# Optimization experiments

Hardware: AMD Instinct MI355X
Metric: run time of the kernel (lower is better)

Reference implementation:

```python
import jax, jax.numpy as jnp
import numpy as np

B, A = 4096, 8          # episodes, agents per episode
N = B * A               # total nodes
E = B * A * (A - 1)     # fully-connected directed edges within each group
F_IN, D, H, M, NA = 64, 64, 4, 64, 10  # in_feat, gnn_dim, heads, mem_dim, n_actions
NEG_SLOPE = 0.2
LN_EPS = 1e-5


def _build_edge_index():
    base = np.arange(A)
    s = np.repeat(base, A)
    d = np.tile(base, A)
    keep = s != d
    s, d = s[keep], d[keep]                       # [A*(A-1)]
    offs = (np.arange(B) * A)[:, None]
    src = (offs + s[None, :]).reshape(-1)
    dst = (offs + d[None, :]).reshape(-1)
    return jnp.asarray(np.stack([src, dst]), dtype=jnp.int32)  # [2, E]


def setup_inputs() -> dict:
    key = jax.random.key(0)
    ks = jax.random.split(key, 16)
    sc = 0.05
    return {
        "x": jax.random.normal(ks[0], (N, F_IN), jnp.float32),
        "edge_attr": jax.random.normal(ks[1], (E, 3), jnp.float32),
        "hidden": jax.random.normal(ks[2], (N, M), jnp.float32) * sc,
        "edge_index": _build_edge_index(),
        # GATv2 params
        "Wl": jax.random.normal(ks[3], (H * D, F_IN), jnp.float32) * sc,
        "bl": jnp.zeros((H * D,), jnp.float32),
        "Wr": jax.random.normal(ks[4], (H * D, F_IN), jnp.float32) * sc,
        "br": jnp.zeros((H * D,), jnp.float32),
        "We": jax.random.normal(ks[5], (H * D, 3), jnp.float32) * sc,
        "be": jnp.zeros((H * D,), jnp.float32),
        "att": jax.random.normal(ks[6], (H, D), jnp.float32) * sc,
        "bias_g": jnp.zeros((D,), jnp.float32),
        # GRUCell params (gate order r,z,n as in torch)
        "W_ih": jax.random.normal(ks[7], (3 * M, D), jnp.float32) * sc,
        "W_hh": jax.random.normal(ks[8], (3 * M, M), jnp.float32) * sc,
        "b_ih": jnp.zeros((3 * M,), jnp.float32),
        "b_hh": jnp.zeros((3 * M,), jnp.float32),
        # LayerNorm + output Linear
        "ln_g": jnp.ones((M,), jnp.float32),
        "ln_b": jnp.zeros((M,), jnp.float32),
        "Wq": jax.random.normal(ks[9], (NA, M), jnp.float32) * sc,
        "bq": jnp.zeros((NA,), jnp.float32),
    }


def reference(x, edge_attr, hidden, edge_index, Wl, bl, Wr, br, We, be, att,
              bias_g, W_ih, W_hh, b_ih, b_hh, ln_g, ln_b, Wq, bq):
    src, dst = edge_index[0], edge_index[1]
    # GATv2Conv (concat=False -> mean over heads), share_weights=False
    xl = (x @ Wl.T + bl).reshape(N, H, D)          # source projection
    xr = (x @ Wr.T + br).reshape(N, H, D)          # target projection
    ee = (edge_attr @ We.T + be).reshape(E, H, D)  # edge embedding
    m = jax.nn.leaky_relu(xl[src] + xr[dst] + ee, NEG_SLOPE)  # [E,H,D]
    logits = jnp.einsum('ehd,hd->eh', m, att)                  # [E,H]
    lmax = jax.ops.segment_max(logits, dst, num_segments=N)    # [N,H]
    ex = jnp.exp(logits - lmax[dst])
    denom = jax.ops.segment_sum(ex, dst, num_segments=N)       # [N,H]
    alpha = ex / denom[dst]                                    # softmax per target
    agg = jax.ops.segment_sum(alpha[:, :, None] * xl[src], dst, num_segments=N)  # [N,H,D]
    h_gnn = jax.nn.relu(agg.mean(axis=1) + bias_g)             # [N,D]
    # GRUCell
    gi = h_gnn @ W_ih.T + b_ih
    gh = hidden @ W_hh.T + b_hh
    ir, iz, inn = jnp.split(gi, 3, axis=-1)
    hr, hz, hn = jnp.split(gh, 3, axis=-1)
    r = jax.nn.sigmoid(ir + hr)
    z = jax.nn.sigmoid(iz + hz)
    n = jnp.tanh(inn + r * hn)
    h = (1.0 - z) * n + z * hidden                              # [N,M]
    # LayerNorm + Linear head
    mu = h.mean(axis=-1, keepdims=True)
    var = ((h - mu) ** 2).mean(axis=-1, keepdims=True)
    hln = (h - mu) / jnp.sqrt(var + LN_EPS) * ln_g + ln_b
    q = hln @ Wq.T + bq                                         # [N,NA]
    return q, h
```

## Files before the change

kernel.cpp:

```cpp
#include <hip/hip_runtime.h>

typedef unsigned short u16;
typedef unsigned int u32;
typedef __attribute__((ext_vector_type(8))) short bf16x8;
typedef __attribute__((ext_vector_type(4))) float f32x4;
typedef _Float16 f16;
typedef __attribute__((ext_vector_type(2))) f16 h2;
typedef __attribute__((ext_vector_type(8))) f16 h8;

#define NAG 8
#define NAGB 16
#define FIN 64
#define MDIM 64
#define NACT 10
#define EPG 56
#define NTOT 32768
#define ABP 72
#define XLS 272
#define XHS 64

#define U_XR  4352
#define U_RZ  0
#define U_HNH 4224
#define U_INB 5312
#define U_HG  6400
#define U_LN  3200

__device__ __forceinline__ float b2f(u16 u) {
  return __uint_as_float(((unsigned int)u) << 16);
}
__device__ __forceinline__ u16 f2b(float f) {
  unsigned int x = __float_as_uint(f);
  unsigned int r = x + 0x7fffu + ((x >> 16) & 1u);
  return (u16)(r >> 16);
}
__device__ __forceinline__ u16 f2h(float f) {
  f16 h = (f16)f; u16 u; __builtin_memcpy(&u, &h, 2); return u;
}
__device__ __forceinline__ float h2f(u16 u) {
  f16 h; __builtin_memcpy(&h, &u, 2); return (float)h;
}
__device__ __forceinline__ u32 pkh2(float a, float b) {
#if __has_builtin(__builtin_amdgcn_cvt_pkrtz)
  auto r = __builtin_amdgcn_cvt_pkrtz(a, b);
  u32 u; __builtin_memcpy(&u, &r, 4); return u;
#else
  return (u32)f2h(a) | ((u32)f2h(b) << 16);
#endif
}

union H8u { h8 v; h2 p[4]; };

__device__ __forceinline__ h8 lrelu8(h8 m) {
  h8 s = m * (f16)0.2f;
#if __has_builtin(__builtin_elementwise_max)
  return __builtin_elementwise_max(m, s);
#else
  h8 r;
#pragma unroll
  for (int i = 0; i < 8; i++) r[i] = (m[i] > s[i]) ? m[i] : s[i];
  return r;
#endif
}

#if __has_builtin(__builtin_amdgcn_fdot2)
__device__ __forceinline__ float dotacc(h2 a, h2 b, float c) {
  return __builtin_amdgcn_fdot2(a, b, c, false);
}
#else
__device__ __forceinline__ float dotacc(h2 a, h2 b, float c) {
  c += (float)a[0] * (float)b[0];
  c += (float)a[1] * (float)b[1];
  return c;
}
#endif

__global__ __launch_bounds__(256) void prep_weights(
    const float* __restrict__ Wl, const float* __restrict__ Wr,
    const float* __restrict__ Wih, const float* __restrict__ Whh,
    u16* __restrict__ wsB)
{
  const int idx = blockIdx.x * 256 + threadIdx.x;
  if (idx >= 56 * 2 * 64) return;
  const int L  = idx & 63;
  const int ks = (idx >> 6) & 1;
  const int T  = idx >> 7;
  const float* W; int row0;
  if      (T < 16) { W = Wl;  row0 = T * 16; }
  else if (T < 32) { W = Wr;  row0 = (T - 16) * 16; }
  else if (T < 44) { W = Wih; row0 = (T - 32) * 16; }
  else             { W = Whh; row0 = (T - 44) * 16; }
  const int row = row0 + (L & 15);
  const int k0  = ks * 32 + (L >> 4) * 8;
  u16 v[8];
#pragma unroll
  for (int j = 0; j < 8; j++) v[j] = f2b(W[row * 64 + k0 + j]);
  *(bf16x8*)(wsB + (size_t)idx * 8) = *(bf16x8*)v;
}

__global__ __launch_bounds__(256, 7) void gnn_rnn_kernel(
    const float* __restrict__ x, const float* __restrict__ edge_attr,
    const float* __restrict__ hidden,
    const float* __restrict__ bl, const float* __restrict__ br,
    const float* __restrict__ We, const float* __restrict__ be,
    const float* __restrict__ att, const float* __restrict__ bias_g,
    const float* __restrict__ b_ih, const float* __restrict__ b_hh,
    const float* __restrict__ ln_g, const float* __restrict__ ln_b,
    const float* __restrict__ Wq, const float* __restrict__ bq,
    const u16* __restrict__ wsB,
    float* __restrict__ d_out)
{
  __shared__ __align__(16) char uraw[17408];
  __shared__ __align__(16) u16 s_al[NAGB * 4 * 8];
  __shared__ __align__(16) u16 s_hidb[NAGB * ABP];
  __shared__ __align__(16) u16 s_w0h[256], s_w1h[256], s_w2h[256], s_atth[256];

  u16*   uXL  = (u16*)uraw;
  u16*   uXR  = (u16*)uraw + U_XR;
  u16*   uHn  = (u16*)uraw + U_HNH;
  u16*   uInn = (u16*)uraw + U_INB;
  u16*   s_hgb = (u16*)uraw + U_HG;
  float* uF   = (float*)uraw;
  u16*   s_xb = (u16*)uraw;

  const int t = threadIdx.x;
  const int b = blockIdx.x;
  const int L = t & 63;
  const int w = t >> 6;
  const int q = L >> 4;

  {
    const float* xb = x + b * (NAGB * FIN);
    const float* hb = hidden + b * (NAGB * MDIM);
#pragma unroll
    for (int i = t; i < NAGB * FIN; i += 256) {
      const int a = i >> 6, m = i & 63;
      s_xb[a * ABP + m] = f2b(xb[i]);
      s_hidb[a * ABP + m] = f2b(hb[i]);
    }
    s_w0h[t]  = f2h(We[t * 3]);
    s_w1h[t]  = f2h(We[t * 3 + 1]);
    s_w2h[t]  = f2h(We[t * 3 + 2]);
    s_atth[t] = f2h(att[t]);
  }
  float ea00 = 0.f, ea01 = 0.f, ea02 = 0.f, ea10 = 0.f, ea11 = 0.f, ea12 = 0.f;
  if (L < EPG) {
    const float* eb = edge_attr + b * (2 * EPG * 3) + L * 3;
    ea00 = eb[0]; ea01 = eb[1]; ea02 = eb[2];
    ea10 = eb[EPG * 3]; ea11 = eb[EPG * 3 + 1]; ea12 = eb[EPG * 3 + 2];
  }
  __syncthreads();

  {
    const int arow = L & 15;
    bf16x8 af0 = *(const bf16x8*)&s_xb[arow * ABP + q * 8];
    bf16x8 af1 = *(const bf16x8*)&s_xb[arow * ABP + 32 + q * 8];
    __syncthreads();
    const bf16x8* wsBv = (const bf16x8*)wsB;
#pragma unroll 4
    for (int i = 0; i < 8; i++) {
      const int T = w * 8 + i;
      f32x4 acc = {0.f, 0.f, 0.f, 0.f};
      acc = __builtin_amdgcn_mfma_f32_16x16x32_bf16(wsBv[(T * 2 + 0) * 64 + L], af0, acc, 0, 0, 0);
      acc = __builtin_amdgcn_mfma_f32_16x16x32_bf16(wsBv[(T * 2 + 1) * 64 + L], af1, acc, 0, 0, 0);
      const int agent = L & 15;
      const int Tm = T & 15;
      const int h = Tm >> 2;
      const int gcb = Tm * 16 + q * 4;
      const int d0 = (Tm & 3) * 16 + q * 4;
      f32x4 bias4;
      if (T < 16) bias4 = *(const f32x4*)(bl + gcb);
      else        bias4 = *(const f32x4*)(br + gcb) + *(const f32x4*)(be + gcb);
      f32x4 v = acc + bias4;
      u32 pk2[2] = { pkh2(v[0], v[1]), pkh2(v[2], v[3]) };
      u16* dst = (T < 16 ? uXL : uXR) + agent * XLS + h * XHS + d0;
      *(uint2*)dst = *(uint2*)pk2;
    }
  }
  __syncthreads();

  {
    const int h = w;
    if (L < EPG) {
      const int e = L;
      const int s = e / 7, k = e % 7;
      const int j = k + (k >= s ? 1 : 0);
      const f16 a00 = (f16)ea00, a01 = (f16)ea01, a02 = (f16)ea02;
      const f16 a10 = (f16)ea10, a11 = (f16)ea11, a12 = (f16)ea12;
      const u16* xlp0 = uXL + s * XLS + h * XHS;
      const u16* xrp0 = uXR + j * XLS + h * XHS;
      const u16* xlp1 = uXL + (8 + s) * XLS + h * XHS;
      const u16* xrp1 = uXR + (8 + j) * XLS + h * XHS;
      const u16* w0p = s_w0h + h * 64;
      const u16* w1p = s_w1h + h * 64;
      const u16* w2p = s_w2h + h * 64;
      const u16* atp = s_atth + h * 64;
      float lgA0 = 0.f, lgB0 = 0.f, lgA1 = 0.f, lgB1 = 0.f;
#pragma unroll 2
      for (int kq = 0; kq < 8; kq++) {
        H8u w0, w1, w2, at, x0, r0, x1, r1, m0, m1;
        w0.v = *(const h8*)(w0p + kq * 8);
        w1.v = *(const h8*)(w1p + kq * 8);
        w2.v = *(const h8*)(w2p + kq * 8);
        at.v = *(const h8*)(atp + kq * 8);
        x0.v = *(const h8*)(xlp0 + kq * 8);
        r0.v = *(const h8*)(xrp0 + kq * 8);
        x1.v = *(const h8*)(xlp1 + kq * 8);
        r1.v = *(const h8*)(xrp1 + kq * 8);
        m0.v = x0.v + r0.v + w0.v * a00 + w1.v * a01 + w2.v * a02;
        m0.v = lrelu8(m0.v);
        m1.v = x1.v + r1.v + w0.v * a10 + w1.v * a11 + w2.v * a12;
        m1.v = lrelu8(m1.v);
        lgA0 = dotacc(m0.p[0], at.p[0], lgA0);
        lgB0 = dotacc(m0.p[1], at.p[1], lgB0);
        lgA0 = dotacc(m0.p[2], at.p[2], lgA0);
        lgB0 = dotacc(m0.p[3], at.p[3], lgB0);
        lgA1 = dotacc(m1.p[0], at.p[0], lgA1);
        lgB1 = dotacc(m1.p[1], at.p[1], lgB1);
        lgA1 = dotacc(m1.p[2], at.p[2], lgA1);
        lgB1 = dotacc(m1.p[3], at.p[3], lgB1);
      }
      s_al[((    j) * 4 + h) * 8 + s] = f2h(__expf(lgA0 + lgB0));
      s_al[((8 + j) * 4 + h) * 8 + s] = f2h(__expf(lgA1 + lgB1));
    } else {
      const int j2 = L - EPG;
      s_al[((    j2) * 4 + w) * 8 + j2] = 0;
      s_al[((8 + j2) * 4 + w) * 8 + j2] = 0;
    }
  }
  __syncthreads();

  {
    const int ep = t >> 7, jj = (t >> 4) & 7, dq = t & 15;
    const int a16 = ep * 8 + jj;
    float acc[4] = {0.f, 0.f, 0.f, 0.f};
#pragma unroll
    for (int h = 0; h < 4; h++) {
      H8u av;
      av.v = *(const h8*)&s_al[(a16 * 4 + h) * 8];
      float den = 0.f;
      float ah[4] = {0.f, 0.f, 0.f, 0.f};
#pragma unroll
      for (int s = 0; s < 8; s++) {
        float al = (float)av.v[s];
        den += al;
        const u16* xp = uXL + (ep * 8 + s) * XLS + h * XHS + dq * 4;
        ushort4 xv = *(const ushort4*)xp;
        ah[0] += al * h2f(xv.x);
        ah[1] += al * h2f(xv.y);
        ah[2] += al * h2f(xv.z);
        ah[3] += al * h2f(xv.w);
      }
      const float inv = 1.f / den;
#pragma unroll
      for (int c = 0; c < 4; c++) acc[c] += ah[c] * inv;
    }
    const f32x4 bg = *(const f32x4*)(bias_g + dq * 4);
    u16 pk[4];
#pragma unroll
    for (int c = 0; c < 4; c++) {
      float v = acc[c] * 0.25f + bg[c];
      pk[c] = f2b(v > 0.f ? v : 0.f);
    }
    *(uint2*)&s_hgb[a16 * ABP + dq * 4] = *(uint2*)pk;
  }
  __syncthreads();

  {
    const int arow = L & 15;
    bf16x8 ag0 = *(const bf16x8*)&s_hgb[arow * ABP + q * 8];
    bf16x8 ag1 = *(const bf16x8*)&s_hgb[arow * ABP + 32 + q * 8];
    bf16x8 ah0 = *(const bf16x8*)&s_hidb[arow * ABP + q * 8];
    bf16x8 ah1 = *(const bf16x8*)&s_hidb[arow * ABP + 32 + q * 8];
    const bf16x8* wsBv = (const bf16x8*)wsB;
#pragma unroll
    for (int i = 0; i < 3; i++) {
      const int T6 = w * 3 + i;
      const int Tg = 32 + T6, Th = 44 + T6;
      f32x4 acci = {0.f, 0.f, 0.f, 0.f};
      acci = __builtin_amdgcn_mfma_f32_16x16x32_bf16(wsBv[(Tg * 2 + 0) * 64 + L], ag0, acci, 0, 0, 0);
      acci = __builtin_amdgcn_mfma_f32_16x16x32_bf16(wsBv[(Tg * 2 + 1) * 64 + L], ag1, acci, 0, 0, 0);
      f32x4 acch = {0.f, 0.f, 0.f, 0.f};
      acch = __builtin_amdgcn_mfma_f32_16x16x32_bf16(wsBv[(Th * 2 + 0) * 64 + L], ah0, acch, 0, 0, 0);
      acch = __builtin_amdgcn_mfma_f32_16x16x32_bf16(wsBv[(Th * 2 + 1) * 64 + L], ah1, acch, 0, 0, 0);
      const int agent = L & 15;
      const int gcb = T6 * 16 + q * 4;
      if (T6 < 8) {
        f32x4 bsum = *(const f32x4*)(b_ih + gcb) + *(const f32x4*)(b_hh + gcb);
        f32x4 v = acci + acch + bsum;
        *(f32x4*)&uF[U_RZ + agent * 132 + gcb] = v;
      } else {
        f32x4 vi = acci + *(const f32x4*)(b_ih + gcb);
        f32x4 vh = acch + *(const f32x4*)(b_hh + gcb);
        const int off = agent * 68 + (gcb - 128);
        u32 pi[2] = { pkh2(vi[0], vi[1]), pkh2(vi[2], vi[3]) };
        u32 ph[2] = { pkh2(vh[0], vh[1]), pkh2(vh[2], vh[3]) };
        *(uint2*)&uInn[off] = *(uint2*)pi;
        *(uint2*)&uHn[off]  = *(uint2*)ph;
      }
    }
  }
  __syncthreads();

  {
    const float lng = ln_g[L];
    const float lnb = ln_b[L];
#pragma unroll
    for (int rr = 0; rr < 4; rr++) {
      const int a = w + rr * 4, m = L;
      float rz_r = uF[U_RZ + a * 132 + m];
      float rz_z = uF[U_RZ + a * 132 + 64 + m];
      float inn  = h2f(uInn[a * 68 + m]);
      float hn   = h2f(uHn[a * 68 + m]);
      float hid  = b2f(s_hidb[a * ABP + m]);
      float r = 1.f / (1.f + __expf(-rz_r));
      float z = 1.f / (1.f + __expf(-rz_z));
      float xg = inn + r * hn;
      xg = fminf(fmaxf(xg, -20.f), 20.f);
      float e2 = __expf(2.f * xg);
      float n = (e2 - 1.f) / (e2 + 1.f);
      float hv = (1.f - z) * n + z * hid;
      d_out[NTOT * NACT + (b * NAGB + a) * MDIM + m] = hv;
      float sum = hv, sq = hv * hv;
#pragma unroll
      for (int off = 1; off < 64; off <<= 1) {
        sum += __shfl_xor(sum, off, 64);
        sq  += __shfl_xor(sq,  off, 64);
      }
      float mu  = sum * (1.f / 64.f);
      float var = sq * (1.f / 64.f) - mu * mu;
      var = var > 0.f ? var : 0.f;
      uF[U_LN + a * 68 + m] = (hv - mu) * rsqrtf(var + 1e-5f) * lng + lnb;
    }
  }
  __syncthreads();

  if (t < NAGB * NACT) {
    const int a = t / NACT, o = t % NACT;
    float acc = bq[o];
    const float4* lv = (const float4*)(uF + U_LN + a * 68);
    const float4* wv = (const float4*)(Wq + o * 64);
#pragma unroll 4
    for (int kq = 0; kq < 16; kq++) {
      float4 l4 = lv[kq], w4 = wv[kq];
      acc += l4.x * w4.x + l4.y * w4.y + l4.z * w4.z + l4.w * w4.w;
    }
    d_out[(b * NAGB + a) * NACT + o] = acc;
  }
}

extern "C" void kernel_launch(void* const* d_in, const int* in_sizes, int n_in,
                              void* d_out, int out_size, void* d_ws, size_t ws_size,
                              hipStream_t stream) {
  const int N  = in_sizes[0] / FIN;
  const int Bn = N / NAGB;
  u16* wsB = (u16*)d_ws;

  prep_weights<<<28, 256, 0, stream>>>(
      (const float*)d_in[4],
      (const float*)d_in[6],
      (const float*)d_in[12],
      (const float*)d_in[13],
      wsB);

  gnn_rnn_kernel<<<Bn, 256, 0, stream>>>(
      (const float*)d_in[0], (const float*)d_in[1], (const float*)d_in[2],
      (const float*)d_in[5],
      (const float*)d_in[7],
      (const float*)d_in[8],
      (const float*)d_in[9],
      (const float*)d_in[10],
      (const float*)d_in[11],
      (const float*)d_in[14],
      (const float*)d_in[15],
      (const float*)d_in[16], (const float*)d_in[17],
      (const float*)d_in[18], (const float*)d_in[19],
      wsB, (float*)d_out);
}
```

Before: 144.3 us.

## Use MFMA for Q head, packed fp16 aggregation, and padded xl stride

Replaces the scalar per-thread Q-head dot product with two f16 MFMA instructions on one wavefront, using a Wq tile pre-packed to fp16 in the weight prep kernel and LayerNorm output stored as fp16. The attention-weighted aggregation now accumulates in packed half2 arithmetic instead of fp32 scalar FMAs. The xl shared-memory row stride is padded to reduce bank conflicts, and the occupancy hint drops from 7 to 6 blocks per CU. Together these aim to cut ALU and LDS cost, at the price of fp16 accumulation error in the aggregation and more shared memory per block.

```diff
diff --git a/kernel.cpp b/kernel.cpp
--- a/kernel.cpp
+++ b/kernel.cpp
@@ -16,15 +16,17 @@
 #define EPG 56
 #define NTOT 32768
 #define ABP 72
-#define XLS 272
-#define XHS 64
-
-#define U_XR  4352
+#define XLS 296
+#define XHS 72
+
+#define U_XR  4736
 #define U_RZ  0
 #define U_HNH 4224
 #define U_INB 5312
 #define U_HG  6400
-#define U_LN  3200
+#define U_LNH 6400
+
+#define WQOFF 57344
 
 __device__ __forceinline__ float b2f(u16 u) {
   return __uint_as_float(((unsigned int)u) << 16);
@@ -78,27 +80,36 @@
 __global__ __launch_bounds__(256) void prep_weights(
     const float* __restrict__ Wl, const float* __restrict__ Wr,
     const float* __restrict__ Wih, const float* __restrict__ Whh,
+    const float* __restrict__ Wq,
     u16* __restrict__ wsB)
 {
   const int idx = blockIdx.x * 256 + threadIdx.x;
-  if (idx >= 56 * 2 * 64) return;
+  if (idx >= 57 * 2 * 64) return;
   const int L  = idx & 63;
   const int ks = (idx >> 6) & 1;
   const int T  = idx >> 7;
-  const float* W; int row0;
-  if      (T < 16) { W = Wl;  row0 = T * 16; }
-  else if (T < 32) { W = Wr;  row0 = (T - 16) * 16; }
-  else if (T < 44) { W = Wih; row0 = (T - 32) * 16; }
-  else             { W = Whh; row0 = (T - 44) * 16; }
-  const int row = row0 + (L & 15);
-  const int k0  = ks * 32 + (L >> 4) * 8;
   u16 v[8];
-#pragma unroll
-  for (int j = 0; j < 8; j++) v[j] = f2b(W[row * 64 + k0 + j]);
+  if (T < 56) {
+    const float* W; int row0;
+    if      (T < 16) { W = Wl;  row0 = T * 16; }
+    else if (T < 32) { W = Wr;  row0 = (T - 16) * 16; }
+    else if (T < 44) { W = Wih; row0 = (T - 32) * 16; }
+    else             { W = Whh; row0 = (T - 44) * 16; }
+    const int row = row0 + (L & 15);
+    const int k0  = ks * 32 + (L >> 4) * 8;
+#pragma unroll
+    for (int j = 0; j < 8; j++) v[j] = f2b(W[row * 64 + k0 + j]);
+  } else {
+    const int row = L & 15;
+    const int k0  = ks * 32 + (L >> 4) * 8;
+#pragma unroll
+    for (int j = 0; j < 8; j++)
+      v[j] = (row < NACT) ? f2h(Wq[row * 64 + k0 + j]) : (u16)0;
+  }
   *(bf16x8*)(wsB + (size_t)idx * 8) = *(bf16x8*)v;
 }
 
-__global__ __launch_bounds__(256, 7) void gnn_rnn_kernel(
+__global__ __launch_bounds__(256, 6) void gnn_rnn_kernel(
     const float* __restrict__ x, const float* __restrict__ edge_attr,
     const float* __restrict__ hidden,
     const float* __restrict__ bl, const float* __restrict__ br,
@@ -110,7 +121,7 @@
     const u16* __restrict__ wsB,
     float* __restrict__ d_out)
 {
-  __shared__ __align__(16) char uraw[17408];
+  __shared__ __align__(16) char uraw[18944];
   __shared__ __align__(16) u16 s_al[NAGB * 4 * 8];
   __shared__ __align__(16) u16 s_hidb[NAGB * ABP];
   __shared__ __align__(16) u16 s_w0h[256], s_w1h[256], s_w2h[256], s_atth[256];
@@ -120,6 +131,7 @@
   u16*   uHn  = (u16*)uraw + U_HNH;
   u16*   uInn = (u16*)uraw + U_INB;
   u16*   s_hgb = (u16*)uraw + U_HG;
+  u16*   uLnH = (u16*)uraw + U_LNH;
   float* uF   = (float*)uraw;
   u16*   s_xb = (u16*)uraw;
 
@@ -238,22 +250,27 @@
     for (int h = 0; h < 4; h++) {
       H8u av;
       av.v = *(const h8*)&s_al[(a16 * 4 + h) * 8];
-      float den = 0.f;
-      float ah[4] = {0.f, 0.f, 0.f, 0.f};
+      h2 d2 = (av.p[0] + av.p[1]) + (av.p[2] + av.p[3]);
+      float den = (float)d2[0] + (float)d2[1];
+      h2 ah0 = {(f16)0.f, (f16)0.f};
+      h2 ah1 = {(f16)0.f, (f16)0.f};
 #pragma unroll
       for (int s = 0; s < 8; s++) {
-        float al = (float)av.v[s];
-        den += al;
         const u16* xp = uXL + (ep * 8 + s) * XLS + h * XHS + dq * 4;
-        ushort4 xv = *(const ushort4*)xp;
-        ah[0] += al * h2f(xv.x);
-        ah[1] += al * h2f(xv.y);
-        ah[2] += al * h2f(xv.z);
-        ah[3] += al * h2f(xv.w);
+        uint2 xv = *(const uint2*)xp;
+        h2 x01, x23;
+        __builtin_memcpy(&x01, &xv.x, 4);
+        __builtin_memcpy(&x23, &xv.y, 4);
+        f16 al = av.v[s];
+        h2 al2 = {al, al};
+        ah0 += al2 * x01;
+        ah1 += al2 * x23;
       }
       const float inv = 1.f / den;
-#pragma unroll
-      for (int c = 0; c < 4; c++) acc[c] += ah[c] * inv;
+      acc[0] += (float)ah0[0] * inv;
+      acc[1] += (float)ah0[1] * inv;
+      acc[2] += (float)ah1[0] * inv;
+      acc[3] += (float)ah1[1] * inv;
     }
     const f32x4 bg = *(const f32x4*)(bias_g + dq * 4);
     u16 pk[4];
@@ -330,22 +347,28 @@
       float mu  = sum * (1.f / 64.f);
       float var = sq * (1.f / 64.f) - mu * mu;
       var = var > 0.f ? var : 0.f;
-      uF[U_LN + a * 68 + m] = (hv - mu) * rsqrtf(var + 1e-5f) * lng + lnb;
-    }
-  }
-  __syncthreads();
-
-  if (t < NAGB * NACT) {
-    const int a = t / NACT, o = t % NACT;
-    float acc = bq[o];
-    const float4* lv = (const float4*)(uF + U_LN + a * 68);
-    const float4* wv = (const float4*)(Wq + o * 64);
-#pragma unroll 4
-    for (int kq = 0; kq < 16; kq++) {
-      float4 l4 = lv[kq], w4 = wv[kq];
-      acc += l4.x * w4.x + l4.y * w4.y + l4.z * w4.z + l4.w * w4.w;
-    }
-    d_out[(b * NAGB + a) * NACT + o] = acc;
+      uLnH[a * ABP + m] = f2h((hv - mu) * rsqrtf(var + 1e-5f) * lng + lnb);
+    }
+  }
+  __syncthreads();
+
+  if (w == 0) {
+    const int agent = L & 15;
+    const u16* wq = wsB + WQOFF;
+    h8 wq0, wq1, ln0, ln1;
+    wq0 = *(const h8*)(wq + (size_t)(0 * 64 + L) * 8);
+    wq1 = *(const h8*)(wq + (size_t)(1 * 64 + L) * 8);
+    ln0 = *(const h8*)(uLnH + agent * ABP + q * 8);
+    ln1 = *(const h8*)(uLnH + agent * ABP + 32 + q * 8);
+    f32x4 acc = {0.f, 0.f, 0.f, 0.f};
+    acc = __builtin_amdgcn_mfma_f32_16x16x32_f16(wq0, ln0, acc, 0, 0, 0);
+    acc = __builtin_amdgcn_mfma_f32_16x16x32_f16(wq1, ln1, acc, 0, 0, 0);
+    float* qout = d_out + ((size_t)b * NAGB + agent) * NACT;
+#pragma unroll
+    for (int r = 0; r < 4; r++) {
+      const int o = q * 4 + r;
+      if (o < NACT) qout[o] = acc[r] + bq[o];
+    }
   }
 }
 
@@ -356,11 +379,12 @@
   const int Bn = N / NAGB;
   u16* wsB = (u16*)d_ws;
 
-  prep_weights<<<28, 256, 0, stream>>>(
+  prep_weights<<<29, 256, 0, stream>>>(
       (const float*)d_in[4],
       (const float*)d_in[6],
       (const float*)d_in[12],
       (const float*)d_in[13],
+      (const float*)d_in[18],
       wsB);
 
   gnn_rnn_kernel<<<Bn, 256, 0, stream>>>(
```

Measured after the change: 135.7 us. 6.0% less time.
